# Kernel optimization log

Measured on AMD Instinct MI355X. Metric: run time of the kernel, lower is better.

## Reference

```python
import jax, jax.numpy as jnp
import numpy as np

B, S, IN, OUT = 4, 2048, 4096, 4096


def setup_inputs() -> dict:
    key = jax.random.key(0)
    k1, k2 = jax.random.split(key, 2)
    x = jax.random.normal(k1, (B, S, IN), dtype=jnp.float32)
    # Materialize the quantized weight the way bitsandbytes int8_vectorwise_quant does:
    # per-output-row absmax (SCB) and int8 codes CB = round(W * 127 / absmax_row).
    Wf = jax.random.normal(k2, (OUT, IN), dtype=jnp.float32) * 0.02
    absmax = jnp.max(jnp.abs(Wf), axis=1)  # [OUT]
    CB = jnp.round(Wf * (127.0 / absmax)[:, None]).astype(jnp.int8)  # [OUT, IN]
    SCB = absmax.astype(jnp.float32)  # [OUT], per-row absmax scale
    return {"x": x, "CB": CB, "SCB": SCB}


def reference(x, CB, SCB):
    # LLM.int8()-style forward (has_fp16_weights=False, no outlier split needed for
    # well-behaved activations): dynamic row-wise int8 quantization of x, int8 GEMM
    # accumulated in int32, then dequant by (absmax_x/127) * (SCB/127).
    absmax_x = jnp.max(jnp.abs(x), axis=-1, keepdims=True)  # [B,S,1]
    sx = absmax_x / 127.0
    xq = jnp.round(x / sx).astype(jnp.int8)  # [B,S,IN]
    acc = jnp.einsum("bsk,ok->bso", xq, CB, preferred_element_type=jnp.int32)
    y = acc.astype(jnp.float32) * sx * (SCB / 127.0)[None, None, :]  # [B,S,OUT]
    return y
```

## Files before the change

### kernel.cpp

```cpp
#include <hip/hip_runtime.h>
#include <stdint.h>

static constexpr int Mtot = 8192;
static constexpr int Ntot = 4096;
static constexpr int Ktot = 4096;

using i32x4 = __attribute__((ext_vector_type(4))) int;

#define GLD16(gptr, lptr)                                                                   \
  __builtin_amdgcn_global_load_lds((const __attribute__((address_space(1))) void*)(gptr),   \
                                   (__attribute__((address_space(3))) void*)(lptr), 16, 0, 0)

__global__ __launch_bounds__(256) void pack_cb_kernel(const int* __restrict__ src,
                                                      int8_t* __restrict__ dst) {
  const int idx = blockIdx.x * 256 + threadIdx.x;
  const int4 v = reinterpret_cast<const int4*>(src)[idx];
  const unsigned packed = (unsigned)(v.x & 0xff) | ((unsigned)(v.y & 0xff) << 8) |
                          ((unsigned)(v.z & 0xff) << 16) | ((unsigned)(v.w & 0xff) << 24);
  reinterpret_cast<unsigned*>(dst)[idx] = packed;
}

__global__ __launch_bounds__(256) void quant_x_kernel(const float* __restrict__ x,
                                                      int8_t* __restrict__ xq,
                                                      float* __restrict__ sx) {
  const int row = blockIdx.x;
  const float4* xr = reinterpret_cast<const float4*>(x + (size_t)row * Ktot);
  float4 v[4];
  float am = 0.f;
#pragma unroll
  for (int i = 0; i < 4; ++i) {
    v[i] = xr[threadIdx.x + i * 256];
    am = fmaxf(am, fmaxf(fmaxf(fabsf(v[i].x), fabsf(v[i].y)),
                         fmaxf(fabsf(v[i].z), fabsf(v[i].w))));
  }
#pragma unroll
  for (int off = 32; off > 0; off >>= 1) am = fmaxf(am, __shfl_xor(am, off));
  __shared__ float wmax[4];
  if ((threadIdx.x & 63) == 0) wmax[threadIdx.x >> 6] = am;
  __syncthreads();
  am = fmaxf(fmaxf(wmax[0], wmax[1]), fmaxf(wmax[2], wmax[3]));
  const float inv = 127.0f / am;
  if (threadIdx.x == 0) sx[row] = am * (1.0f / 127.0f);
  unsigned* dq = reinterpret_cast<unsigned*>(xq + (size_t)row * Ktot);
#pragma unroll
  for (int i = 0; i < 4; ++i) {
    const int q0 = (int)rintf(v[i].x * inv);
    const int q1 = (int)rintf(v[i].y * inv);
    const int q2 = (int)rintf(v[i].z * inv);
    const int q3 = (int)rintf(v[i].w * inv);
    dq[threadIdx.x + i * 256] = (unsigned)(q0 & 0xff) | ((unsigned)(q1 & 0xff) << 8) |
                                ((unsigned)(q2 & 0xff) << 16) | ((unsigned)(q3 & 0xff) << 24);
  }
}

__global__ __launch_bounds__(256) void gemm_i8_kernel(const int8_t* __restrict__ A,
                                                      const int8_t* __restrict__ B,
                                                      const float* __restrict__ sx,
                                                      const float* __restrict__ scb,
                                                      float* __restrict__ C) {
  constexpr int BK = 64;
  __shared__ int8_t As[128 * BK];
  __shared__ int8_t Bs[128 * BK];

  const int tid = threadIdx.x;
  const int lane = tid & 63;
  const int wid = tid >> 6;
  const int m0 = blockIdx.y * 128;
  const int n0 = blockIdx.x * 128;
  const int wm = (wid >> 1) * 64;
  const int wn = (wid & 1) * 64;

  const int srow = tid >> 2;
  const int scol = (tid & 3) * 16;
  const int8_t* Ag0 = A + (size_t)(m0 + srow) * Ktot + scol;
  const int8_t* Ag1 = A + (size_t)(m0 + 64 + srow) * Ktot + scol;
  const int8_t* Bg0 = B + (size_t)(n0 + srow) * Ktot + scol;
  const int8_t* Bg1 = B + (size_t)(n0 + 64 + srow) * Ktot + scol;
  int8_t* lA0 = &As[tid * 16];
  int8_t* lA1 = &As[4096 + tid * 16];
  int8_t* lB0 = &Bs[tid * 16];
  int8_t* lB1 = &Bs[4096 + tid * 16];

  i32x4 acc[4][4];
#pragma unroll
  for (int i = 0; i < 4; ++i)
#pragma unroll
    for (int j = 0; j < 4; ++j) acc[i][j] = (i32x4)0;

  const int mrow = lane & 15;
  const int kq = (lane >> 4) * 16;

  for (int kt = 0; kt < Ktot; kt += BK) {
    GLD16(Ag0 + kt, lA0);
    GLD16(Ag1 + kt, lA1);
    GLD16(Bg0 + kt, lB0);
    GLD16(Bg1 + kt, lB1);
    __syncthreads();

    i32x4 af[4], bf[4];
#pragma unroll
    for (int i = 0; i < 4; ++i)
      af[i] = *reinterpret_cast<const i32x4*>(&As[(wm + i * 16 + mrow) * BK + kq]);
#pragma unroll
    for (int j = 0; j < 4; ++j)
      bf[j] = *reinterpret_cast<const i32x4*>(&Bs[(wn + j * 16 + mrow) * BK + kq]);
#pragma unroll
    for (int i = 0; i < 4; ++i)
#pragma unroll
      for (int j = 0; j < 4; ++j)
        acc[i][j] = __builtin_amdgcn_mfma_i32_16x16x64_i8(af[i], bf[j], acc[i][j], 0, 0, 0);
    __syncthreads();
  }

  const int col = lane & 15;
  const int rbase = (lane >> 4) * 4;
#pragma unroll
  for (int i = 0; i < 4; ++i) {
    const int gmb = m0 + wm + i * 16 + rbase;
    float sm[4];
#pragma unroll
    for (int r = 0; r < 4; ++r) sm[r] = sx[gmb + r];
#pragma unroll
    for (int j = 0; j < 4; ++j) {
      const int gn = n0 + wn + j * 16 + col;
      const float snv = scb[gn] * (1.0f / 127.0f);
#pragma unroll
      for (int r = 0; r < 4; ++r)
        C[(size_t)(gmb + r) * Ntot + gn] = (float)acc[i][j][r] * sm[r] * snv;
    }
  }
}

extern "C" void kernel_launch(void* const* d_in, const int* in_sizes, int n_in,
                              void* d_out, int out_size, void* d_ws, size_t ws_size,
                              hipStream_t stream) {
  const float* x = (const float*)d_in[0];
  const int* CB32 = (const int*)d_in[1];
  const float* SCB = (const float*)d_in[2];
  float* out = (float*)d_out;

  int8_t* xq = (int8_t*)d_ws;
  int8_t* cb8 = (int8_t*)d_ws + (size_t)Mtot * Ktot;
  float* sx = (float*)((int8_t*)d_ws + (size_t)Mtot * Ktot + (size_t)Ntot * Ktot);

  pack_cb_kernel<<<(Ntot * Ktot / 4) / 256, 256, 0, stream>>>(CB32, cb8);
  quant_x_kernel<<<Mtot, 256, 0, stream>>>(x, xq, sx);
  dim3 grid(Ntot / 128, Mtot / 128);
  gemm_i8_kernel<<<grid, 256, 0, stream>>>(xq, cb8, sx, SCB, out);
}
```

Baseline: 415.6 us.

## Rework int8 GEMM into 256x256 double-buffered swizzled tiles and fuse prep kernels

The GEMM tile grows from 128x128 with BK=64 to 256x256 with BK=128 and 512 threads, and each warp now computes a 128x64 sub-tile. The next K slice is double-buffered into LDS while the current one is multiplied. Loads use an XOR-swizzled LDS layout to avoid bank conflicts, MFMA phases get s_setprio, and a block-index swizzle is added for L2 locality. The CB pack and x quantisation kernels are merged into one launch. The goal is more data reuse per LDS byte and less global-load latency and launch overhead, at the cost of 128KB of LDS per block (low occupancy) and more registers.

```diff
diff --git a/kernel.cpp b/kernel.cpp
--- a/kernel.cpp
+++ b/kernel.cpp
@@ -11,19 +11,21 @@
   __builtin_amdgcn_global_load_lds((const __attribute__((address_space(1))) void*)(gptr),   \
                                    (__attribute__((address_space(3))) void*)(lptr), 16, 0, 0)
 
-__global__ __launch_bounds__(256) void pack_cb_kernel(const int* __restrict__ src,
-                                                      int8_t* __restrict__ dst) {
-  const int idx = blockIdx.x * 256 + threadIdx.x;
-  const int4 v = reinterpret_cast<const int4*>(src)[idx];
-  const unsigned packed = (unsigned)(v.x & 0xff) | ((unsigned)(v.y & 0xff) << 8) |
-                          ((unsigned)(v.z & 0xff) << 16) | ((unsigned)(v.w & 0xff) << 24);
-  reinterpret_cast<unsigned*>(dst)[idx] = packed;
-}
-
-__global__ __launch_bounds__(256) void quant_x_kernel(const float* __restrict__ x,
-                                                      int8_t* __restrict__ xq,
-                                                      float* __restrict__ sx) {
-  const int row = blockIdx.x;
+__global__ __launch_bounds__(256) void prep_kernel(const int* __restrict__ cb32,
+                                                   int8_t* __restrict__ cb8,
+                                                   const float* __restrict__ x,
+                                                   int8_t* __restrict__ xq,
+                                                   float* __restrict__ sx) {
+  __shared__ float wmax[4];
+  if (blockIdx.x < 16384) {
+    const int idx = blockIdx.x * 256 + threadIdx.x;
+    const int4 v = reinterpret_cast<const int4*>(cb32)[idx];
+    const unsigned packed = (unsigned)(v.x & 0xff) | ((unsigned)(v.y & 0xff) << 8) |
+                            ((unsigned)(v.z & 0xff) << 16) | ((unsigned)(v.w & 0xff) << 24);
+    reinterpret_cast<unsigned*>(cb8)[idx] = packed;
+    return;
+  }
+  const int row = blockIdx.x - 16384;
   const float4* xr = reinterpret_cast<const float4*>(x + (size_t)row * Ktot);
   float4 v[4];
   float am = 0.f;
@@ -35,7 +37,6 @@
   }
 #pragma unroll
   for (int off = 32; off > 0; off >>= 1) am = fmaxf(am, __shfl_xor(am, off));
-  __shared__ float wmax[4];
   if ((threadIdx.x & 63) == 0) wmax[threadIdx.x >> 6] = am;
   __syncthreads();
   am = fmaxf(fmaxf(wmax[0], wmax[1]), fmaxf(wmax[2], wmax[3]));
@@ -53,80 +54,132 @@
   }
 }
 
-__global__ __launch_bounds__(256) void gemm_i8_kernel(const int8_t* __restrict__ A,
-                                                      const int8_t* __restrict__ B,
-                                                      const float* __restrict__ sx,
-                                                      const float* __restrict__ scb,
-                                                      float* __restrict__ C) {
-  constexpr int BK = 64;
-  __shared__ int8_t As[128 * BK];
-  __shared__ int8_t Bs[128 * BK];
+__global__ __launch_bounds__(512, 2) void gemm_i8_kernel(const int8_t* __restrict__ A,
+                                                         const int8_t* __restrict__ B,
+                                                         const float* __restrict__ sx,
+                                                         const float* __restrict__ scb,
+                                                         float* __restrict__ C) {
+  constexpr int BK = 128;
+  constexpr int NT = Ktot / BK;
+  __shared__ __align__(16) int8_t lds[131072];
 
   const int tid = threadIdx.x;
   const int lane = tid & 63;
   const int wid = tid >> 6;
-  const int m0 = blockIdx.y * 128;
-  const int n0 = blockIdx.x * 128;
-  const int wm = (wid >> 1) * 64;
-  const int wn = (wid & 1) * 64;
-
-  const int srow = tid >> 2;
-  const int scol = (tid & 3) * 16;
-  const int8_t* Ag0 = A + (size_t)(m0 + srow) * Ktot + scol;
-  const int8_t* Ag1 = A + (size_t)(m0 + 64 + srow) * Ktot + scol;
-  const int8_t* Bg0 = B + (size_t)(n0 + srow) * Ktot + scol;
-  const int8_t* Bg1 = B + (size_t)(n0 + 64 + srow) * Ktot + scol;
-  int8_t* lA0 = &As[tid * 16];
-  int8_t* lA1 = &As[4096 + tid * 16];
-  int8_t* lB0 = &Bs[tid * 16];
-  int8_t* lB1 = &Bs[4096 + tid * 16];
-
-  i32x4 acc[4][4];
-#pragma unroll
-  for (int i = 0; i < 4; ++i)
-#pragma unroll
-    for (int j = 0; j < 4; ++j) acc[i][j] = (i32x4)0;
-
-  const int mrow = lane & 15;
-  const int kq = (lane >> 4) * 16;
-
-  for (int kt = 0; kt < Ktot; kt += BK) {
-    GLD16(Ag0 + kt, lA0);
-    GLD16(Ag1 + kt, lA1);
-    GLD16(Bg0 + kt, lB0);
-    GLD16(Bg1 + kt, lB1);
-    __syncthreads();
-
-    i32x4 af[4], bf[4];
-#pragma unroll
-    for (int i = 0; i < 4; ++i)
-      af[i] = *reinterpret_cast<const i32x4*>(&As[(wm + i * 16 + mrow) * BK + kq]);
-#pragma unroll
-    for (int j = 0; j < 4; ++j)
-      bf[j] = *reinterpret_cast<const i32x4*>(&Bs[(wn + j * 16 + mrow) * BK + kq]);
-#pragma unroll
-    for (int i = 0; i < 4; ++i)
-#pragma unroll
-      for (int j = 0; j < 4; ++j)
-        acc[i][j] = __builtin_amdgcn_mfma_i32_16x16x64_i8(af[i], bf[j], acc[i][j], 0, 0, 0);
+
+  const int wg = (int)blockIdx.x;
+  const int wgs = (wg & 7) * 64 + (wg >> 3);
+  const int m0 = (wgs >> 4) * 256;
+  const int n0 = (wgs & 15) * 256;
+
+  const int wm = (wid >> 2) * 128;
+  const int wn = (wid & 3) * 64;
+
+  const int srow = tid >> 3;
+  const int scol = ((tid & 7) * 16) ^ ((srow & 7) << 4);
+  const int8_t* gA = A + (size_t)(m0 + srow) * Ktot + scol;
+  const int8_t* gB = B + (size_t)(n0 + srow) * Ktot + scol;
+
+  const int l15 = lane & 15;
+  const int lc0 = ((lane >> 4) * 16) ^ ((lane & 7) << 4);
+  const int aOff = (wm + l15) * 128 + lc0;
+  const int bOff = 65536 + (wn + l15) * 128 + lc0;
+
+  i32x4 acc[8][4];
+#pragma unroll
+  for (int f = 0; f < 8; ++f)
+#pragma unroll
+    for (int g = 0; g < 4; ++g) acc[f][g] = (i32x4)0;
+
+#pragma unroll
+  for (int i = 0; i < 4; ++i) {
+    GLD16(gA + (size_t)(i * 64) * Ktot, &lds[i * 8192 + tid * 16]);
+    GLD16(gB + (size_t)(i * 64) * Ktot, &lds[65536 + i * 8192 + tid * 16]);
+  }
+  __syncthreads();
+
+#pragma unroll 2
+  for (int t = 0; t < NT; ++t) {
+    const int bo = (t & 1) * 32768;
+    const int so = ((t & 1) ^ 1) * 32768;
+    i32x4 a[4], b[4];
+
+#pragma unroll
+    for (int f = 0; f < 4; ++f) a[f] = *(const i32x4*)&lds[bo + aOff + f * 2048];
+#pragma unroll
+    for (int g = 0; g < 4; ++g) b[g] = *(const i32x4*)&lds[bo + bOff + g * 2048];
+    if (t + 1 < NT) {
+      const size_t kn = (size_t)(t + 1) * BK;
+#pragma unroll
+      for (int i = 0; i < 4; ++i) {
+        GLD16(gA + kn + (size_t)(i * 64) * Ktot, &lds[so + i * 8192 + tid * 16]);
+        GLD16(gB + kn + (size_t)(i * 64) * Ktot, &lds[65536 + so + i * 8192 + tid * 16]);
+      }
+    }
+    __builtin_amdgcn_s_barrier();
+    __builtin_amdgcn_s_setprio(1);
+#pragma unroll
+    for (int f = 0; f < 4; ++f)
+#pragma unroll
+      for (int g = 0; g < 4; ++g)
+        acc[f][g] = __builtin_amdgcn_mfma_i32_16x16x64_i8(a[f], b[g], acc[f][g], 0, 0, 0);
+    __builtin_amdgcn_s_setprio(0);
+    __builtin_amdgcn_s_barrier();
+
+#pragma unroll
+    for (int f = 0; f < 4; ++f) a[f] = *(const i32x4*)&lds[bo + aOff + (f + 4) * 2048];
+    __builtin_amdgcn_s_barrier();
+    __builtin_amdgcn_s_setprio(1);
+#pragma unroll
+    for (int f = 0; f < 4; ++f)
+#pragma unroll
+      for (int g = 0; g < 4; ++g)
+        acc[f + 4][g] = __builtin_amdgcn_mfma_i32_16x16x64_i8(a[f], b[g], acc[f + 4][g], 0, 0, 0);
+    __builtin_amdgcn_s_setprio(0);
+    __builtin_amdgcn_s_barrier();
+
+#pragma unroll
+    for (int f = 0; f < 4; ++f) a[f] = *(const i32x4*)&lds[bo + (aOff ^ 64) + f * 2048];
+#pragma unroll
+    for (int g = 0; g < 4; ++g) b[g] = *(const i32x4*)&lds[bo + (bOff ^ 64) + g * 2048];
+    __builtin_amdgcn_s_barrier();
+    __builtin_amdgcn_s_setprio(1);
+#pragma unroll
+    for (int f = 0; f < 4; ++f)
+#pragma unroll
+      for (int g = 0; g < 4; ++g)
+        acc[f][g] = __builtin_amdgcn_mfma_i32_16x16x64_i8(a[f], b[g], acc[f][g], 0, 0, 0);
+    __builtin_amdgcn_s_setprio(0);
+    __builtin_amdgcn_s_barrier();
+
+#pragma unroll
+    for (int f = 0; f < 4; ++f) a[f] = *(const i32x4*)&lds[bo + (aOff ^ 64) + (f + 4) * 2048];
+    __builtin_amdgcn_s_barrier();
+    __builtin_amdgcn_s_setprio(1);
+#pragma unroll
+    for (int f = 0; f < 4; ++f)
+#pragma unroll
+      for (int g = 0; g < 4; ++g)
+        acc[f + 4][g] = __builtin_amdgcn_mfma_i32_16x16x64_i8(a[f], b[g], acc[f + 4][g], 0, 0, 0);
+    __builtin_amdgcn_s_setprio(0);
     __syncthreads();
   }
 
   const int col = lane & 15;
   const int rbase = (lane >> 4) * 4;
 #pragma unroll
-  for (int i = 0; i < 4; ++i) {
-    const int gmb = m0 + wm + i * 16 + rbase;
+  for (int f = 0; f < 8; ++f) {
+    const int gmb = m0 + wm + f * 16 + rbase;
     float sm[4];
 #pragma unroll
     for (int r = 0; r < 4; ++r) sm[r] = sx[gmb + r];
 #pragma unroll
-    for (int j = 0; j < 4; ++j) {
-      const int gn = n0 + wn + j * 16 + col;
+    for (int g = 0; g < 4; ++g) {
+      const int gn = n0 + wn + g * 16 + col;
       const float snv = scb[gn] * (1.0f / 127.0f);
 #pragma unroll
       for (int r = 0; r < 4; ++r)
-        C[(size_t)(gmb + r) * Ntot + gn] = (float)acc[i][j][r] * sm[r] * snv;
+        C[(size_t)(gmb + r) * Ntot + gn] = (float)acc[f][g][r] * sm[r] * snv;
     }
   }
 }
@@ -143,8 +196,6 @@
   int8_t* cb8 = (int8_t*)d_ws + (size_t)Mtot * Ktot;
   float* sx = (float*)((int8_t*)d_ws + (size_t)Mtot * Ktot + (size_t)Ntot * Ktot);
 
-  pack_cb_kernel<<<(Ntot * Ktot / 4) / 256, 256, 0, stream>>>(CB32, cb8);
-  quant_x_kernel<<<Mtot, 256, 0, stream>>>(x, xq, sx);
-  dim3 grid(Ntot / 128, Mtot / 128);
-  gemm_i8_kernel<<<grid, 256, 0, stream>>>(xq, cb8, sx, SCB, out);
+  prep_kernel<<<16384 + Mtot, 256, 0, stream>>>(CB32, cb8, x, xq, sx);
+  gemm_i8_kernel<<<512, 512, 0, stream>>>(xq, cb8, sx, SCB, out);
 }
```

After: 386.0 us. -7.1%, faster.
